# Kernel optimization log

Hardware: AMD Instinct MI355X
Metric: run time of the kernel (lower is better)

The kernel has to match this reference:

```python
import jax, jax.numpy as jnp
import numpy as np

HEADS = 4

def setup_inputs() -> dict:
    B, L, D = 4, 2048, 256
    key = jax.random.key(0)
    k1, k2, k3, k4, k5, k6 = jax.random.split(key, 6)
    return {
        "atten": jax.random.normal(k1, (B, L, L), dtype=jnp.float32),
        "value": jax.random.normal(k2, (B, L, D), dtype=jnp.float32),
        "mask": jax.random.uniform(k3, (B, 1, L, L), dtype=jnp.float32),
        "padding_mask": jax.random.randint(k4, (B, L, L), 0, 2, dtype=jnp.int32),
        "Wv": jax.random.normal(k5, (D, D), dtype=jnp.float32) * 0.02,
        "bv": jnp.zeros((D,), dtype=jnp.float32),
        "Wo": jax.random.normal(k6, (D, D), dtype=jnp.float32) * 0.02,
        "bo": jnp.zeros((D,), dtype=jnp.float32),
    }

def reference(atten, value, mask, padding_mask, Wv, bv, Wo, bo):
    B, L, D = value.shape
    H = HEADS
    dk = D // H
    # to_value: Linear then split heads. N == 1 (value.unsqueeze(1) in torch).
    v = value @ Wv + bv                                   # (B, L, D)
    v = v.reshape(B, 1, L, H, dk).transpose(0, 3, 1, 2, 4)  # (B, H, N=1, L, dk)
    # externally supplied attention logits, two sequential masked fills
    a = atten[:, None, :, :]                              # (B, 1, L, L)
    a = jnp.where(mask < 0.5, jnp.finfo(a.dtype).min, a)
    a = jnp.where(padding_mask[:, None, :, :] == 0, -jnp.inf, a)
    a = jax.nn.softmax(a, axis=-1)                        # (B, 1, L, L)
    # dropout is identity in eval mode
    # einsum 'bhij,bhnjk->bhnik' with h=1 on a broadcast across H heads of v
    out = jnp.einsum('bij,bhnjk->bhnik', a[:, 0], v)      # (B, H, 1, L, dk)
    out = out.transpose(0, 2, 3, 1, 4).reshape(B, 1, L, D)
    out = out @ Wo + bo                                   # (B, 1, L, D)
    return out
```

## Files before the change

kernel.cpp:

```cpp
#include <hip/hip_runtime.h>
#include <hip/hip_bf16.h>
#include <math.h>

#define L 2048
#define D 256
#define NEG_FLT_MAX (-3.402823466e38f)

typedef __attribute__((ext_vector_type(8))) short bf16x8;
typedef __attribute__((ext_vector_type(4))) float f32x4;
typedef __attribute__((ext_vector_type(4))) int i32x4;

__device__ __forceinline__ unsigned short f2bf(float f) {
    union { float f; unsigned int u; } v; v.f = f;
    unsigned int r = v.u + 0x7FFFu + ((v.u >> 16) & 1u);
    return (unsigned short)(r >> 16);
}

__global__ __launch_bounds__(256, 4) void prep_kernel(
    const float* __restrict__ value, const float* __restrict__ Wv,
    const float* __restrict__ bv, const float* __restrict__ Wo,
    unsigned short* __restrict__ Vt, unsigned short* __restrict__ Wot) {
    const int tid = threadIdx.x;
    const int wave = tid >> 6, lane = tid & 63;
    const int lm = lane & 15, q = lane >> 4;
    const int rh = wave >> 1;
    const int nh = wave & 1;
    const int m0 = blockIdx.x * 32;
    const int n0 = blockIdx.y * 64;

    __shared__ __align__(16) unsigned short Wlds[64][264];

    {
        int bid = blockIdx.y * 256 + blockIdx.x;
        if (tid < 64) {
            int e = bid * 64 + tid;
            int k = e >> 8, n = e & 255;
            Wot[n * 256 + k] = f2bf(Wo[k * 256 + n]);
        }
    }

    {
        int krow = tid >> 4;
        int nrel = (tid & 15) * 4;
#pragma unroll
        for (int p = 0; p < 16; p++) {
            int k = p * 16 + krow;
            f32x4 w = *reinterpret_cast<const f32x4*>(Wv + (size_t)k * 256 + n0 + nrel);
            Wlds[nrel + 0][k] = f2bf(w[0]);
            Wlds[nrel + 1][k] = f2bf(w[1]);
            Wlds[nrel + 2][k] = f2bf(w[2]);
            Wlds[nrel + 3][k] = f2bf(w[3]);
        }
    }
    __syncthreads();

    const int nl0 = nh * 32 + lm;
    const int nl1 = nh * 32 + 16 + lm;
    const int arow = m0 + rh * 16 + lm;

    f32x4 acc[2];
    acc[0] = (f32x4)(0.f); acc[1] = (f32x4)(0.f);

    const float* ap = value + (size_t)arow * 256;
    f32x4 pa0 = *reinterpret_cast<const f32x4*>(ap + q * 8);
    f32x4 pa1 = *reinterpret_cast<const f32x4*>(ap + q * 8 + 4);

    for (int k0 = 0; k0 < 256; k0 += 32) {
        f32x4 a0 = pa0, a1 = pa1;
        if (k0 < 224) {
            int kq = k0 + 32 + q * 8;
            pa0 = *reinterpret_cast<const f32x4*>(ap + kq);
            pa1 = *reinterpret_cast<const f32x4*>(ap + kq + 4);
        }
        bf16x8 b0 = *reinterpret_cast<const bf16x8*>(&Wlds[nl0][k0 + q * 8]);
        bf16x8 b1 = *reinterpret_cast<const bf16x8*>(&Wlds[nl1][k0 + q * 8]);
        bf16x8 afr;
#pragma unroll
        for (int e = 0; e < 4; e++) afr[e] = (short)f2bf(a0[e]);
#pragma unroll
        for (int e = 0; e < 4; e++) afr[4 + e] = (short)f2bf(a1[e]);
        acc[0] = __builtin_amdgcn_mfma_f32_16x16x32_bf16(afr, b0, acc[0], 0, 0, 0);
        acc[1] = __builtin_amdgcn_mfma_f32_16x16x32_bf16(afr, b1, acc[1], 0, 0, 0);
    }

    int mrow = m0 + rh * 16 + q * 4;
    int b = mrow >> 11;
    int j = mrow & 2047;
#pragma unroll
    for (int nf = 0; nf < 2; nf++) {
        int n = n0 + nh * 32 + nf * 16 + lm;
        float bias_n = bv[n];
        const f32x4& a = acc[nf];
        unsigned short* dst = Vt + (size_t)b * (D * L) + (size_t)n * L + j;
        ushort4 pk;
        pk.x = f2bf(a[0] + bias_n);
        pk.y = f2bf(a[1] + bias_n);
        pk.z = f2bf(a[2] + bias_n);
        pk.w = f2bf(a[3] + bias_n);
        *reinterpret_cast<ushort4*>(dst) = pk;
    }
}

__global__ __launch_bounds__(256, 2) void attn_kernel(
    const float* __restrict__ atten, const float* __restrict__ mask,
    const int* __restrict__ pad, const unsigned short* __restrict__ Vt,
    const unsigned short* __restrict__ Wot, const float* __restrict__ bo,
    float* __restrict__ out) {
    const int g = blockIdx.x;
    const int b = g >> 7;
    const int i0 = (g & 127) * 16;
    const int tid = threadIdx.x;
    const int wave = tid >> 6, lane = tid & 63;
    const int lm = lane & 15, q = lane >> 4;
    const int r = tid >> 4;
    const int c = (tid & 15) * 8;

    __shared__ __align__(16) unsigned short Plds[2][16][136];
    __shared__ __align__(16) unsigned short A_lds[16][264];
    __shared__ float l_lds[16];

    f32x4 acc[4];
#pragma unroll
    for (int nf = 0; nf < 4; nf++) acc[nf] = (f32x4)(0.f);
    float lsum = 0.f;

    const size_t rowoff = ((size_t)(b * L + i0 + r)) * L + c;
    const float* at_p = atten + rowoff;
    const float* mk_p = mask + rowoff;
    const int*   pd_p = pad + rowoff;
    const unsigned short* vt_b = Vt + (size_t)b * (D * L);

    f32x4 pa0 = *reinterpret_cast<const f32x4*>(at_p);
    f32x4 pa1 = *reinterpret_cast<const f32x4*>(at_p + 4);
    f32x4 pm0 = *reinterpret_cast<const f32x4*>(mk_p);
    f32x4 pm1 = *reinterpret_cast<const f32x4*>(mk_p + 4);
    i32x4 pp0 = *reinterpret_cast<const i32x4*>(pd_p);
    i32x4 pp1 = *reinterpret_cast<const i32x4*>(pd_p + 4);

    for (int jt = 0; jt < 16; jt++) {
        const int j0 = jt * 128;
        bf16x8 bfr[4][4];
#pragma unroll
        for (int kk = 0; kk < 4; kk++)
#pragma unroll
            for (int nf = 0; nf < 4; nf++) {
                int n = wave * 64 + nf * 16 + lm;
                bfr[kk][nf] = *reinterpret_cast<const bf16x8*>(
                    vt_b + (size_t)n * L + j0 + kk * 32 + q * 8);
            }
        f32x4 a0 = pa0, a1 = pa1, k0 = pm0, k1 = pm1;
        i32x4 p0 = pp0, p1 = pp1;
        if (jt < 15) {
            pa0 = *reinterpret_cast<const f32x4*>(at_p + j0 + 128);
            pa1 = *reinterpret_cast<const f32x4*>(at_p + j0 + 132);
            pm0 = *reinterpret_cast<const f32x4*>(mk_p + j0 + 128);
            pm1 = *reinterpret_cast<const f32x4*>(mk_p + j0 + 132);
            pp0 = *reinterpret_cast<const i32x4*>(pd_p + j0 + 128);
            pp1 = *reinterpret_cast<const i32x4*>(pd_p + j0 + 132);
        }
        bf16x8 pk;
#pragma unroll
        for (int e = 0; e < 4; e++) {
            float sv = (k0[e] < 0.5f) ? NEG_FLT_MAX : a0[e];
            sv = (p0[e] == 0) ? -INFINITY : sv;
            float pv = __expf(sv);
            lsum += pv;
            pk[e] = (short)f2bf(pv);
            float sw = (k1[e] < 0.5f) ? NEG_FLT_MAX : a1[e];
            sw = (p1[e] == 0) ? -INFINITY : sw;
            float pw = __expf(sw);
            lsum += pw;
            pk[4 + e] = (short)f2bf(pw);
        }
        const int par = jt & 1;
        *reinterpret_cast<bf16x8*>(&Plds[par][r][c]) = pk;
        __syncthreads();

#pragma unroll
        for (int kk = 0; kk < 4; kk++) {
            bf16x8 afr = *reinterpret_cast<const bf16x8*>(
                &Plds[par][lm][kk * 32 + q * 8]);
#pragma unroll
            for (int nf = 0; nf < 4; nf++)
                acc[nf] = __builtin_amdgcn_mfma_f32_16x16x32_bf16(
                    afr, bfr[kk][nf], acc[nf], 0, 0, 0);
        }
    }

    lsum += __shfl_xor(lsum, 1);
    lsum += __shfl_xor(lsum, 2);
    lsum += __shfl_xor(lsum, 4);
    lsum += __shfl_xor(lsum, 8);
    if ((tid & 15) == 0) l_lds[r] = lsum;
    __syncthreads();

    float linv[4];
#pragma unroll
    for (int rg = 0; rg < 4; rg++) linv[rg] = 1.f / l_lds[q * 4 + rg];
#pragma unroll
    for (int nf = 0; nf < 4; nf++) {
        int n = wave * 64 + nf * 16 + lm;
#pragma unroll
        for (int rg = 0; rg < 4; rg++)
            A_lds[q * 4 + rg][n] = f2bf(acc[nf][rg] * linv[rg]);
    }
    __syncthreads();

    f32x4 oacc[4];
#pragma unroll
    for (int nf = 0; nf < 4; nf++) oacc[nf] = (f32x4)(0.f);
    for (int k0 = 0; k0 < 256; k0 += 32) {
        bf16x8 afr = *reinterpret_cast<const bf16x8*>(&A_lds[lm][k0 + q * 8]);
#pragma unroll
        for (int nf = 0; nf < 4; nf++) {
            int n = wave * 64 + nf * 16 + lm;
            bf16x8 bfrW = *reinterpret_cast<const bf16x8*>(
                Wot + (size_t)n * 256 + k0 + q * 8);
            oacc[nf] = __builtin_amdgcn_mfma_f32_16x16x32_bf16(
                afr, bfrW, oacc[nf], 0, 0, 0);
        }
    }
#pragma unroll
    for (int nf = 0; nf < 4; nf++) {
        int n = wave * 64 + nf * 16 + lm;
        float bias_n = bo[n];
#pragma unroll
        for (int rg = 0; rg < 4; rg++)
            out[((size_t)(b * L + i0 + q * 4 + rg)) * 256 + n] = oacc[nf][rg] + bias_n;
    }
}

extern "C" void kernel_launch(void* const* d_in, const int* in_sizes, int n_in,
                              void* d_out, int out_size, void* d_ws, size_t ws_size,
                              hipStream_t stream) {
    (void)in_sizes; (void)n_in; (void)out_size; (void)ws_size;
    const float* atten = (const float*)d_in[0];
    const float* value = (const float*)d_in[1];
    const float* mask  = (const float*)d_in[2];
    const int*   pad   = (const int*)d_in[3];
    const float* Wv    = (const float*)d_in[4];
    const float* bv    = (const float*)d_in[5];
    const float* Wo    = (const float*)d_in[6];
    const float* bo    = (const float*)d_in[7];
    float* out = (float*)d_out;

    char* ws = (char*)d_ws;
    unsigned short* Vt  = (unsigned short*)(ws);
    unsigned short* Wot = (unsigned short*)(ws + 4194304);

    prep_kernel<<<dim3(256, 4), 256, 0, stream>>>(value, Wv, bv, Wo, Vt, Wot);
    attn_kernel<<<512, 256, 0, stream>>>(atten, mask, pad, Vt, Wot, bo, out);
}
```

Before: 254.1 us.

## Split attn kernel into full-row softmax phase then single-sync MFMA phase

The attention kernel now computes the masked exponentials for an entire 16x2048 row block in one streaming pass, storing the bf16 probabilities in a large shared-memory buffer, then runs the P·V MFMA loop with no per-tile barriers. It also remaps block indices so that consecutive blocks are spread across batches. Finally it applies the masks after the exponential (multiplying by zero) rather than before. This is meant to decouple the bandwidth-bound read of atten, mask and pad from the MFMA phase and to remove the 16 barriers. In exchange, the roughly 66KB of shared memory lowers occupancy, and the load and compute phases no longer overlap within a block.

```diff
diff --git a/kernel.cpp b/kernel.cpp
--- a/kernel.cpp
+++ b/kernel.cpp
@@ -4,7 +4,6 @@
 
 #define L 2048
 #define D 256
-#define NEG_FLT_MAX (-3.402823466e38f)
 
 typedef __attribute__((ext_vector_type(8))) short bf16x8;
 typedef __attribute__((ext_vector_type(4))) float f32x4;
@@ -38,7 +37,6 @@
             Wot[n * 256 + k] = f2bf(Wo[k * 256 + n]);
         }
     }
-
     {
         int krow = tid >> 4;
         int nrel = (tid & 15) * 4;
@@ -106,93 +104,79 @@
     const int* __restrict__ pad, const unsigned short* __restrict__ Vt,
     const unsigned short* __restrict__ Wot, const float* __restrict__ bo,
     float* __restrict__ out) {
-    const int g = blockIdx.x;
+    const int bid = blockIdx.x;
+    const int g = (bid & 7) * 64 + (bid >> 3);
     const int b = g >> 7;
     const int i0 = (g & 127) * 16;
     const int tid = threadIdx.x;
     const int wave = tid >> 6, lane = tid & 63;
     const int lm = lane & 15, q = lane >> 4;
-    const int r = tid >> 4;
-    const int c = (tid & 15) * 8;
-
-    __shared__ __align__(16) unsigned short Plds[2][16][136];
+
+    __shared__ __align__(16) unsigned short Plds[16][2056];
     __shared__ __align__(16) unsigned short A_lds[16][264];
     __shared__ float l_lds[16];
 
+    {
+        const int r = tid >> 4;
+        const int c4 = (tid & 15) * 4;
+        const size_t rowbase = ((size_t)(b * L + i0 + r)) * L + c4;
+        const float* at_r = atten + rowbase;
+        const float* mk_r = mask + rowbase;
+        const int*   pd_r = pad + rowbase;
+        float lsum = 0.f;
+#pragma unroll 2
+        for (int jt = 0; jt < 8; jt++) {
+            const int jb = jt * 256;
+            f32x4 av[4], mv[4];
+            i32x4 pv[4];
+#pragma unroll
+            for (int s = 0; s < 4; s++) {
+                av[s] = *reinterpret_cast<const f32x4*>(at_r + jb + s * 64);
+                mv[s] = *reinterpret_cast<const f32x4*>(mk_r + jb + s * 64);
+                pv[s] = *reinterpret_cast<const i32x4*>(pd_r + jb + s * 64);
+            }
+#pragma unroll
+            for (int s = 0; s < 4; s++) {
+                float pe[4];
+#pragma unroll
+                for (int e = 0; e < 4; e++) {
+                    float p = __expf(av[s][e]);
+                    p = (mv[s][e] < 0.5f) ? 0.f : p;
+                    p = (pv[s][e] == 0) ? 0.f : p;
+                    pe[e] = p;
+                }
+                lsum += (pe[0] + pe[1]) + (pe[2] + pe[3]);
+                ushort4 pk;
+                pk.x = f2bf(pe[0]); pk.y = f2bf(pe[1]);
+                pk.z = f2bf(pe[2]); pk.w = f2bf(pe[3]);
+                *reinterpret_cast<ushort4*>(&Plds[r][jb + c4 + s * 64]) = pk;
+            }
+        }
+        lsum += __shfl_xor(lsum, 1);
+        lsum += __shfl_xor(lsum, 2);
+        lsum += __shfl_xor(lsum, 4);
+        lsum += __shfl_xor(lsum, 8);
+        if ((tid & 15) == 0) l_lds[r] = lsum;
+    }
+    __syncthreads();
+
     f32x4 acc[4];
 #pragma unroll
     for (int nf = 0; nf < 4; nf++) acc[nf] = (f32x4)(0.f);
-    float lsum = 0.f;
-
-    const size_t rowoff = ((size_t)(b * L + i0 + r)) * L + c;
-    const float* at_p = atten + rowoff;
-    const float* mk_p = mask + rowoff;
-    const int*   pd_p = pad + rowoff;
-    const unsigned short* vt_b = Vt + (size_t)b * (D * L);
-
-    f32x4 pa0 = *reinterpret_cast<const f32x4*>(at_p);
-    f32x4 pa1 = *reinterpret_cast<const f32x4*>(at_p + 4);
-    f32x4 pm0 = *reinterpret_cast<const f32x4*>(mk_p);
-    f32x4 pm1 = *reinterpret_cast<const f32x4*>(mk_p + 4);
-    i32x4 pp0 = *reinterpret_cast<const i32x4*>(pd_p);
-    i32x4 pp1 = *reinterpret_cast<const i32x4*>(pd_p + 4);
-
-    for (int jt = 0; jt < 16; jt++) {
-        const int j0 = jt * 128;
-        bf16x8 bfr[4][4];
-#pragma unroll
-        for (int kk = 0; kk < 4; kk++)
-#pragma unroll
-            for (int nf = 0; nf < 4; nf++) {
-                int n = wave * 64 + nf * 16 + lm;
-                bfr[kk][nf] = *reinterpret_cast<const bf16x8*>(
-                    vt_b + (size_t)n * L + j0 + kk * 32 + q * 8);
-            }
-        f32x4 a0 = pa0, a1 = pa1, k0 = pm0, k1 = pm1;
-        i32x4 p0 = pp0, p1 = pp1;
-        if (jt < 15) {
-            pa0 = *reinterpret_cast<const f32x4*>(at_p + j0 + 128);
-            pa1 = *reinterpret_cast<const f32x4*>(at_p + j0 + 132);
-            pm0 = *reinterpret_cast<const f32x4*>(mk_p + j0 + 128);
-            pm1 = *reinterpret_cast<const f32x4*>(mk_p + j0 + 132);
-            pp0 = *reinterpret_cast<const i32x4*>(pd_p + j0 + 128);
-            pp1 = *reinterpret_cast<const i32x4*>(pd_p + j0 + 132);
-        }
-        bf16x8 pk;
-#pragma unroll
-        for (int e = 0; e < 4; e++) {
-            float sv = (k0[e] < 0.5f) ? NEG_FLT_MAX : a0[e];
-            sv = (p0[e] == 0) ? -INFINITY : sv;
-            float pv = __expf(sv);
-            lsum += pv;
-            pk[e] = (short)f2bf(pv);
-            float sw = (k1[e] < 0.5f) ? NEG_FLT_MAX : a1[e];
-            sw = (p1[e] == 0) ? -INFINITY : sw;
-            float pw = __expf(sw);
-            lsum += pw;
-            pk[4 + e] = (short)f2bf(pw);
-        }
-        const int par = jt & 1;
-        *reinterpret_cast<bf16x8*>(&Plds[par][r][c]) = pk;
-        __syncthreads();
-
-#pragma unroll
-        for (int kk = 0; kk < 4; kk++) {
-            bf16x8 afr = *reinterpret_cast<const bf16x8*>(
-                &Plds[par][lm][kk * 32 + q * 8]);
-#pragma unroll
-            for (int nf = 0; nf < 4; nf++)
-                acc[nf] = __builtin_amdgcn_mfma_f32_16x16x32_bf16(
-                    afr, bfr[kk][nf], acc[nf], 0, 0, 0);
-        }
-    }
-
-    lsum += __shfl_xor(lsum, 1);
-    lsum += __shfl_xor(lsum, 2);
-    lsum += __shfl_xor(lsum, 4);
-    lsum += __shfl_xor(lsum, 8);
-    if ((tid & 15) == 0) l_lds[r] = lsum;
-    __syncthreads();
+
+    const unsigned short* vt_b = Vt + (size_t)b * (D * L) + q * 8;
+    const unsigned short* prow = &Plds[lm][q * 8];
+#pragma unroll 2
+    for (int j0 = 0; j0 < 2048; j0 += 32) {
+        bf16x8 afr = *reinterpret_cast<const bf16x8*>(prow + j0);
+#pragma unroll
+        for (int nf = 0; nf < 4; nf++) {
+            int n = wave * 64 + nf * 16 + lm;
+            bf16x8 bfr = *reinterpret_cast<const bf16x8*>(vt_b + (size_t)n * L + j0);
+            acc[nf] = __builtin_amdgcn_mfma_f32_16x16x32_bf16(
+                afr, bfr, acc[nf], 0, 0, 0);
+        }
+    }
 
     float linv[4];
 #pragma unroll
```

Result: slower. 294.3 us (+15.8%).
